# Optimization experiments

Measured on AMD Instinct MI355X. Metric: run time of the kernel, lower is better.

Reference implementation:

```python
import jax, jax.numpy as jnp
import numpy as np
from jax import lax

DIM = 512
IDIM = 1536
K = 7


def setup_inputs() -> dict:
    key = jax.random.key(0)
    ks = jax.random.split(key, 10)
    B, C, T = 16, DIM, 2048
    x = jax.random.normal(ks[0], (B, C, T), dtype=jnp.float32)
    dw_w = jax.random.normal(ks[1], (DIM, 1, K), dtype=jnp.float32) * (1.0 / np.sqrt(K))
    dw_b = jax.random.normal(ks[2], (DIM,), dtype=jnp.float32) * 0.01
    ln_g = jnp.ones((DIM,), dtype=jnp.float32)
    ln_b = jnp.zeros((DIM,), dtype=jnp.float32)
    w1 = jax.random.normal(ks[3], (IDIM, DIM), dtype=jnp.float32) * (1.0 / np.sqrt(DIM))
    b1 = jax.random.normal(ks[4], (IDIM,), dtype=jnp.float32) * 0.01
    grn_g = jax.random.normal(ks[5], (IDIM,), dtype=jnp.float32) * 0.02
    grn_b = jax.random.normal(ks[6], (IDIM,), dtype=jnp.float32) * 0.02
    w2 = jax.random.normal(ks[7], (DIM, IDIM), dtype=jnp.float32) * (1.0 / np.sqrt(IDIM))
    b2 = jax.random.normal(ks[8], (DIM,), dtype=jnp.float32) * 0.01
    return {"x": x, "dw_w": dw_w, "dw_b": dw_b, "ln_g": ln_g, "ln_b": ln_b,
            "w1": w1, "b1": b1, "grn_g": grn_g, "grn_b": grn_b, "w2": w2, "b2": b2}


def reference(x, dw_w, dw_b, ln_g, ln_b, w1, b1, grn_g, grn_b, w2, b2):
    residual = x  # [B, C, T]
    # depthwise conv1d, padding='same' style (K//2 each side)
    y = lax.conv_general_dilated(
        x, dw_w,
        window_strides=(1,),
        padding=[(K // 2, K // 2)],
        dimension_numbers=("NCH", "OIH", "NCH"),
        feature_group_count=DIM,
    ) + dw_b[None, :, None]
    y = jnp.transpose(y, (0, 2, 1))  # [B, T, C]
    # LayerNorm over channels, eps=1e-6
    mu = jnp.mean(y, axis=-1, keepdims=True)
    var = jnp.mean((y - mu) ** 2, axis=-1, keepdims=True)
    y = (y - mu) * lax.rsqrt(var + 1e-6) * ln_g + ln_b
    # pwconv1 + GELU (exact, erf-based as torch default)
    h = jnp.einsum("btc,ic->bti", y, w1) + b1  # [B, T, IDIM]
    h = jax.nn.gelu(h, approximate=False)
    # GRN: L2 norm over time axis (dim=1), mean over channels
    gx = jnp.sqrt(jnp.sum(h * h, axis=1, keepdims=True))  # [B, 1, IDIM]
    nx = gx / (jnp.mean(gx, axis=-1, keepdims=True) + 1e-6)
    h = grn_g * (h * nx) + grn_b + h
    # pwconv2
    y = jnp.einsum("bti,ci->btc", h, w2) + b2  # [B, T, C]
    y = jnp.transpose(y, (0, 2, 1))  # [B, C, T]
    return residual + y
```

## Files before the change

### kernel.cpp

```cpp
#include <hip/hip_runtime.h>
#include <math.h>

typedef unsigned short u16;
typedef unsigned int u32;
typedef __bf16 bf16x8_t __attribute__((ext_vector_type(8)));
typedef float f32x4_t __attribute__((ext_vector_type(4)));

__device__ __forceinline__ u16 f2bf(float f) {
  __bf16 b = (__bf16)f;
  return __builtin_bit_cast(u16, b);
}

__device__ __forceinline__ void gld16(const void* g, void* l) {
  __builtin_amdgcn_global_load_lds(
      (const __attribute__((address_space(1))) void*)g,
      (__attribute__((address_space(3))) void*)l, 16, 0, 0);
}

__device__ __forceinline__ float gelu_f(float v) {
  float z = 0.7978845608028654f * v * fmaf(0.044715f, v * v, 1.0f);
  float t = __builtin_amdgcn_exp2f(2.8853900817779268f * z);
  float r = __builtin_amdgcn_rcpf(t + 1.0f);
  return v - v * r;
}

__device__ __forceinline__ int swz8(int bid, int nwg) {
  int cpx = nwg >> 3;
  return (bid & 7) * cpx + (bid >> 3);
}

__global__ __launch_bounds__(256) void cast_kernel(const float* __restrict__ src,
                                                   u16* __restrict__ dst, int n) {
  int i = (blockIdx.x * 256 + threadIdx.x) * 4;
  if (i < n) {
    float4 v = *(const float4*)(src + i);
    uint2 o;
    o.x = (u32)f2bf(v.x) | ((u32)f2bf(v.y) << 16);
    o.y = (u32)f2bf(v.z) | ((u32)f2bf(v.w) << 16);
    *(uint2*)(dst + i) = o;
  }
}

__global__ __launch_bounds__(64) void b2ob_kernel(const float* __restrict__ w2,
                                                  const float* __restrict__ grn_b,
                                                  const float* __restrict__ b2,
                                                  float* __restrict__ out) {
  int c = blockIdx.x;
  int l = threadIdx.x;
  float p = 0.f;
  for (int i = l; i < 1536; i += 64) p += grn_b[i] * w2[(size_t)c * 1536 + i];
  #pragma unroll
  for (int s = 32; s; s >>= 1) p += __shfl_xor(p, s);
  if (l == 0) out[c] = b2[c] + p;
}

__global__ __launch_bounds__(512, 4) void conv_ln_kernel(const float* __restrict__ X,
                                                         const float* __restrict__ Wd,
                                                         const float* __restrict__ bd,
                                                         const float* __restrict__ lng,
                                                         const float* __restrict__ lnb,
                                                         u16* __restrict__ Y) {
  __shared__ float ystage[16 * 516];
  __shared__ float mu_s[16], rs_s[16];

  const int c = threadIdx.x;
  const int b = blockIdx.y;
  const int t0 = blockIdx.x * 64;

  const float* xr = X + ((size_t)b * 512 + c) * 2048;
  float wr[7];
  #pragma unroll
  for (int k = 0; k < 7; ++k) wr[k] = Wd[c * 7 + k];
  const float bdv = bd[c];
  const float lg = lng[c];
  const float lb = lnb[c];

  for (int ch = 0; ch < 4; ++ch) {
    const int tc0 = t0 + ch * 16;
    const int g = tc0 - 4;
    float w[24];
    if (g >= 0 && g + 24 <= 2048) {
      #pragma unroll
      for (int q = 0; q < 6; ++q) {
        float4 v = *(const float4*)(xr + g + q * 4);
        w[q * 4 + 0] = v.x; w[q * 4 + 1] = v.y;
        w[q * 4 + 2] = v.z; w[q * 4 + 3] = v.w;
      }
    } else {
      #pragma unroll
      for (int j = 0; j < 24; ++j) {
        int tt = g + j;
        w[j] = (tt >= 0 && tt < 2048) ? xr[tt] : 0.f;
      }
    }
    float outv[16];
    #pragma unroll
    for (int i = 0; i < 16; ++i) {
      float a = bdv;
      #pragma unroll
      for (int k = 0; k < 7; ++k) a = fmaf(w[i + 1 + k], wr[k], a);
      outv[i] = a;
      ystage[i * 516 + c] = a;
    }
    __syncthreads();
    {
      int r = c >> 5, cl = c & 31;
      float s = 0.f, q = 0.f;
      #pragma unroll
      for (int k = 0; k < 16; ++k) {
        float v = ystage[r * 516 + cl + k * 32];
        s += v; q += v * v;
      }
      #pragma unroll
      for (int m = 16; m; m >>= 1) { s += __shfl_xor(s, m); q += __shfl_xor(q, m); }
      if (cl == 0) {
        float mu = s * (1.f / 512.f);
        float var = q * (1.f / 512.f) - mu * mu;
        mu_s[r] = mu;
        rs_s[r] = rsqrtf(var + 1e-6f);
      }
    }
    __syncthreads();
    #pragma unroll
    for (int i = 0; i < 16; ++i) {
      float v = (outv[i] - mu_s[i]) * rs_s[i] * lg + lb;
      Y[(size_t)(b * 2048 + tc0 + i) * 512 + c] = f2bf(v);
    }
  }
}

__global__ __launch_bounds__(256) void grn_kernel(const float* __restrict__ gsum,
                                                  const float* __restrict__ grn_g,
                                                  float* __restrict__ svec) {
  __shared__ float red[256];
  int b = blockIdx.x, tid = threadIdx.x;
  float gx[6];
  float part = 0.f;
  #pragma unroll
  for (int it = 0; it < 6; ++it) {
    int i = it * 256 + tid;
    gx[it] = sqrtf(gsum[b * 1536 + i]);
    part += gx[it];
  }
  red[tid] = part;
  __syncthreads();
  for (int s = 128; s; s >>= 1) {
    if (tid < s) red[tid] += red[tid + s];
    __syncthreads();
  }
  float inv = 1.0f / (red[0] * (1.f / 1536.f) + 1e-6f);
  #pragma unroll
  for (int it = 0; it < 6; ++it) {
    int i = it * 256 + tid;
    svec[b * 1536 + i] = 1.0f + grn_g[i] * gx[it] * inv;
  }
}

__global__ __launch_bounds__(256) void w2s_kernel(const float* __restrict__ w2,
                                                  const float* __restrict__ svec,
                                                  u16* __restrict__ out) {
  size_t e0 = ((size_t)blockIdx.x * 256 + threadIdx.x) * 8;
  int i = (int)(e0 % 1536);
  size_t bc = e0 / 1536;
  int b = (int)(bc >> 9);
  size_t widx = (bc & 511) * 1536 + i;
  float4 wa = *(const float4*)(w2 + widx);
  float4 wb = *(const float4*)(w2 + widx + 4);
  float4 sa = *(const float4*)(svec + b * 1536 + i);
  float4 sb = *(const float4*)(svec + b * 1536 + i + 4);
  uint4 o;
  o.x = (u32)f2bf(wa.x * sa.x) | ((u32)f2bf(wa.y * sa.y) << 16);
  o.y = (u32)f2bf(wa.z * sa.z) | ((u32)f2bf(wa.w * sa.w) << 16);
  o.z = (u32)f2bf(wb.x * sb.x) | ((u32)f2bf(wb.y * sb.y) << 16);
  o.w = (u32)f2bf(wb.z * sb.z) | ((u32)f2bf(wb.w * sb.w) << 16);
  *(uint4*)(out + e0) = o;
}

template<int KD>
__device__ __forceinline__ void gemm_kloop(const u16* __restrict__ Ag,
                                           const u16* __restrict__ Bg,
                                           u16* lds, int NT,
                                           f32x4_t (&acc)[4][4]) {
  const int tid = threadIdx.x;
  const int l = tid & 63, l15 = l & 15, lq = l >> 4;
  const int w = tid >> 6;
  const int wm = w >> 1, wn = w & 1;
  const int rin = tid >> 3;
  const int cs = ((tid & 7) ^ (rin & 7)) << 3;

  auto STAGE = [&](int buf, int kt) {
    u16* lA = lds + buf * 16384;
    u16* lB = lA + 8192;
    #pragma unroll
    for (int c = 0; c < 4; ++c) {
      gld16(Ag + (size_t)(c * 32 + rin) * KD + kt + cs, lA + (c * 32 + w * 8) * 64);
      gld16(Bg + (size_t)(c * 32 + rin) * KD + kt + cs, lB + (c * 32 + w * 8) * 64);
    }
  };

  STAGE(0, 0);
  __syncthreads();

  for (int S = 0; S < NT; ++S) {
    const int cur = S & 1;
    if (S + 1 < NT) STAGE(cur ^ 1, (S + 1) * 64);
    u16* lA = lds + cur * 16384;
    u16* lB = lA + 8192;
    bf16x8_t af[4][2], bf[4][2];
    #pragma unroll
    for (int f = 0; f < 4; ++f) {
      const int Ra = wm * 64 + f * 16 + l15;
      const int Rb = wn * 64 + f * 16 + l15;
      #pragma unroll
      for (int kk = 0; kk < 2; ++kk) {
        af[f][kk] = *(const bf16x8_t*)(lA + Ra * 64 + (((kk * 4 + lq) ^ (Ra & 7)) << 3));
        bf[f][kk] = *(const bf16x8_t*)(lB + Rb * 64 + (((kk * 4 + lq) ^ (Rb & 7)) << 3));
      }
    }
    #pragma unroll
    for (int i = 0; i < 4; ++i)
      #pragma unroll
      for (int j = 0; j < 4; ++j)
        #pragma unroll
        for (int kk = 0; kk < 2; ++kk)
          acc[i][j] = __builtin_amdgcn_mfma_f32_16x16x32_bf16(af[i][kk], bf[j][kk], acc[i][j], 0, 0, 0);
    __syncthreads();
  }
}

__global__ __launch_bounds__(256) void gemm1_kernel(const u16* __restrict__ A,
                                                    const u16* __restrict__ Bw,
                                                    const float* __restrict__ b1,
                                                    u16* __restrict__ H,
                                                    float* __restrict__ gsum) {
  extern __shared__ __align__(16) u16 lds[];
  const int tid = threadIdx.x;
  const int l = tid & 63, l15 = l & 15, lq = l >> 4;
  const int w = tid >> 6, wm = w >> 1, wn = w & 1;
  const int wg = swz8(blockIdx.x, 3072);
  const int ntile = wg % 12, mtile = wg / 12;
  const int m0 = mtile * 128, n0 = ntile * 128;
  const int bidx = m0 >> 11;

  f32x4_t acc[4][4];
  #pragma unroll
  for (int i = 0; i < 4; ++i)
    #pragma unroll
    for (int j = 0; j < 4; ++j) {
      f32x4_t z = {0.f, 0.f, 0.f, 0.f};
      acc[i][j] = z;
    }

  gemm_kloop<512>(A + (size_t)m0 * 512, Bw + (size_t)n0 * 512, lds, 8, acc);

  float bj[4];
  #pragma unroll
  for (int nf = 0; nf < 4; ++nf) bj[nf] = b1[n0 + wn * 64 + nf * 16 + l15];

  float ss[4] = {0.f, 0.f, 0.f, 0.f};
  #pragma unroll
  for (int mf = 0; mf < 4; ++mf) {
    const int lr = wm * 64 + mf * 16 + lq * 4;
    #pragma unroll
    for (int nf = 0; nf < 4; ++nf) {
      const int cl = wn * 64 + nf * 16 + l15;
      #pragma unroll
      for (int r = 0; r < 4; ++r) {
        float g = gelu_f(acc[mf][nf][r] + bj[nf]);
        ss[nf] += g * g;
        lds[(lr + r) * 130 + cl] = f2bf(g);
      }
    }
  }
  #pragma unroll
  for (int nf = 0; nf < 4; ++nf) {
    float v = ss[nf];
    v += __shfl_xor(v, 16);
    v += __shfl_xor(v, 32);
    if (lq == 0) atomicAdd(&gsum[bidx * 1536 + n0 + wn * 64 + nf * 16 + l15], v);
  }
  __syncthreads();
  #pragma unroll
  for (int it = 0; it < 8; ++it) {
    int idx = it * 256 + tid;
    int row = idx >> 4, ch = idx & 15;
    uint4 v = *(const uint4*)(lds + row * 130 + ch * 8);
    *(uint4*)(H + (size_t)(m0 + row) * 1536 + n0 + ch * 8) = v;
  }
}

__global__ __launch_bounds__(256) void gemm2_kernel(const u16* __restrict__ Hm,
                                                    const u16* __restrict__ W2s,
                                                    const float* __restrict__ b2ob,
                                                    const float* __restrict__ X,
                                                    float* __restrict__ Out) {
  extern __shared__ __align__(16) u16 lds[];
  const int tid = threadIdx.x;
  const int l = tid & 63, l15 = l & 15, lq = l >> 4;
  const int w = tid >> 6, wm = w >> 1, wn = w & 1;
  const int wg = swz8(blockIdx.x, 1024);
  const int ntile = wg & 3, mtile = wg >> 2;
  const int m0 = mtile * 128, n0 = ntile * 128;
  const int bidx = m0 >> 11, t0 = m0 & 2047;

  f32x4_t acc[4][4];
  #pragma unroll
  for (int i = 0; i < 4; ++i)
    #pragma unroll
    for (int j = 0; j < 4; ++j) {
      f32x4_t z = {0.f, 0.f, 0.f, 0.f};
      acc[i][j] = z;
    }

  gemm_kloop<1536>(Hm + (size_t)m0 * 1536,
                   W2s + ((size_t)bidx * 512 + n0) * 1536, lds, 24, acc);

  float* st = (float*)lds;
  for (int half = 0; half < 2; ++half) {
    __syncthreads();
    if (wm == half) {
      #pragma unroll
      for (int mf = 0; mf < 4; ++mf) {
        const int lr = mf * 16 + lq * 4;
        #pragma unroll
        for (int nf = 0; nf < 4; ++nf) {
          const int cl = wn * 64 + nf * 16 + l15;
          #pragma unroll
          for (int r = 0; r < 4; ++r)
            st[(lr + r) * 129 + cl] = acc[mf][nf][r];
        }
      }
    }
    __syncthreads();
    const size_t obase = ((size_t)bidx * 512 + n0) * 2048 + (size_t)(t0 + half * 64 + l);
    #pragma unroll
    for (int cc = 0; cc < 32; ++cc) {
      const int c = w * 32 + cc;
      float v = st[l * 129 + c] + b2ob[n0 + c];
      size_t oi = obase + (size_t)c * 2048;
      Out[oi] = v + X[oi];
    }
  }
}

extern "C" void kernel_launch(void* const* d_in, const int* in_sizes, int n_in,
                              void* d_out, int out_size, void* d_ws, size_t ws_size,
                              hipStream_t stream) {
  const float* x     = (const float*)d_in[0];
  const float* dw_w  = (const float*)d_in[1];
  const float* dw_b  = (const float*)d_in[2];
  const float* ln_g  = (const float*)d_in[3];
  const float* ln_b  = (const float*)d_in[4];
  const float* w1    = (const float*)d_in[5];
  const float* b1    = (const float*)d_in[6];
  const float* grn_g = (const float*)d_in[7];
  const float* grn_b = (const float*)d_in[8];
  const float* w2    = (const float*)d_in[9];
  const float* b2    = (const float*)d_in[10];
  float* out = (float*)d_out;

  u16* y_ln = (u16*)d_ws;
  u16* w2s  = y_ln;
  u16* h    = y_ln + (size_t)32768 * 512;
  u16* w1b  = h + (size_t)32768 * 1536;
  float* gsum = (float*)(w1b + (size_t)1536 * 512);
  float* svec = gsum + 16 * 1536;
  float* b2ob = svec + 16 * 1536;

  (void)hipFuncSetAttribute((const void*)gemm1_kernel,
                            hipFuncAttributeMaxDynamicSharedMemorySize, 65536);
  (void)hipFuncSetAttribute((const void*)gemm2_kernel,
                            hipFuncAttributeMaxDynamicSharedMemorySize, 65536);

  hipMemsetAsync(gsum, 0, 16 * 1536 * sizeof(float), stream);
  cast_kernel<<<768, 256, 0, stream>>>(w1, w1b, 1536 * 512);
  b2ob_kernel<<<512, 64, 0, stream>>>(w2, grn_b, b2, b2ob);
  conv_ln_kernel<<<dim3(32, 16), 512, 0, stream>>>(x, dw_w, dw_b, ln_g, ln_b, y_ln);
  gemm1_kernel<<<3072, 256, 65536, stream>>>(y_ln, w1b, b1, h, gsum);
  grn_kernel<<<16, 256, 0, stream>>>(gsum, grn_g, svec);
  w2s_kernel<<<6144, 256, 0, stream>>>(w2, svec, w2s);
  gemm2_kernel<<<1024, 256, 65536, stream>>>(h, w2s, b2ob, x, out);
}
```

Before: 227.3 us.

## Load GEMM A operand directly into registers and halve LDS footprint

Result: slower. 321.1 us (median of 2 runs) (+41.3%).

```diff
diff --git a/kernel.cpp b/kernel.cpp
--- a/kernel.cpp
+++ b/kernel.cpp
@@ -188,34 +188,41 @@
   const int rin = tid >> 3;
   const int cs = ((tid & 7) ^ (rin & 7)) << 3;
 
-  auto STAGE = [&](int buf, int kt) {
-    u16* lA = lds + buf * 16384;
-    u16* lB = lA + 8192;
-    #pragma unroll
-    for (int c = 0; c < 4; ++c) {
-      gld16(Ag + (size_t)(c * 32 + rin) * KD + kt + cs, lA + (c * 32 + w * 8) * 64);
+  const u16* Aw = Ag + (size_t)(wm * 64 + l15) * KD + lq * 8;
+
+  auto STAGE_B = [&](int buf, int kt) {
+    u16* lB = lds + buf * 8192;
+    #pragma unroll
+    for (int c = 0; c < 4; ++c)
       gld16(Bg + (size_t)(c * 32 + rin) * KD + kt + cs, lB + (c * 32 + w * 8) * 64);
-    }
   };
-
-  STAGE(0, 0);
+  auto LOAD_A = [&](bf16x8_t (&ar)[4][2], int kt) {
+    #pragma unroll
+    for (int f = 0; f < 4; ++f)
+      #pragma unroll
+      for (int kk = 0; kk < 2; ++kk)
+        ar[f][kk] = *(const bf16x8_t*)(Aw + (size_t)(f * 16) * KD + kt + kk * 32);
+  };
+
+  bf16x8_t aP[4][2], aQ[4][2];
+  STAGE_B(0, 0);
+  LOAD_A(aP, 0);
   __syncthreads();
 
-  for (int S = 0; S < NT; ++S) {
-    const int cur = S & 1;
-    if (S + 1 < NT) STAGE(cur ^ 1, (S + 1) * 64);
-    u16* lA = lds + cur * 16384;
-    u16* lB = lA + 8192;
-    bf16x8_t af[4][2], bf[4][2];
-    #pragma unroll
-    for (int f = 0; f < 4; ++f) {
-      const int Ra = wm * 64 + f * 16 + l15;
-      const int Rb = wn * 64 + f * 16 + l15;
-      #pragma unroll
-      for (int kk = 0; kk < 2; ++kk) {
-        af[f][kk] = *(const bf16x8_t*)(lA + Ra * 64 + (((kk * 4 + lq) ^ (Ra & 7)) << 3));
-        bf[f][kk] = *(const bf16x8_t*)(lB + Rb * 64 + (((kk * 4 + lq) ^ (Rb & 7)) << 3));
-      }
+  auto STEP = [&](int S, int cur, bf16x8_t (&aC)[4][2], bf16x8_t (&aN)[4][2]) {
+    const bool pf = (S + 1 < NT);
+    if (pf) {
+      STAGE_B(cur ^ 1, (S + 1) * 64);
+      LOAD_A(aN, (S + 1) * 64);
+    }
+    u16* lB = lds + cur * 8192;
+    bf16x8_t bf[4][2];
+    #pragma unroll
+    for (int g = 0; g < 4; ++g) {
+      const int Rb = wn * 64 + g * 16 + l15;
+      #pragma unroll
+      for (int kk = 0; kk < 2; ++kk)
+        bf[g][kk] = *(const bf16x8_t*)(lB + Rb * 64 + (((kk * 4 + lq) ^ (Rb & 7)) << 3));
     }
     #pragma unroll
     for (int i = 0; i < 4; ++i)
@@ -223,16 +230,21 @@
       for (int j = 0; j < 4; ++j)
         #pragma unroll
         for (int kk = 0; kk < 2; ++kk)
-          acc[i][j] = __builtin_amdgcn_mfma_f32_16x16x32_bf16(af[i][kk], bf[j][kk], acc[i][j], 0, 0, 0);
-    __syncthreads();
-  }
-}
-
-__global__ __launch_bounds__(256) void gemm1_kernel(const u16* __restrict__ A,
-                                                    const u16* __restrict__ Bw,
-                                                    const float* __restrict__ b1,
-                                                    u16* __restrict__ H,
-                                                    float* __restrict__ gsum) {
+          acc[i][j] = __builtin_amdgcn_mfma_f32_16x16x32_bf16(aC[i][kk], bf[j][kk], acc[i][j], 0, 0, 0);
+    __syncthreads();
+  };
+
+  for (int S = 0; S < NT; S += 2) {
+    STEP(S, 0, aP, aQ);
+    STEP(S + 1, 1, aQ, aP);
+  }
+}
+
+__global__ __launch_bounds__(256, 2) void gemm1_kernel(const u16* __restrict__ A,
+                                                       const u16* __restrict__ Bw,
+                                                       const float* __restrict__ b1,
+                                                       u16* __restrict__ H,
+                                                       float* __restrict__ gsum) {
   extern __shared__ __align__(16) u16 lds[];
   const int tid = threadIdx.x;
   const int l = tid & 63, l15 = l & 15, lq = l >> 4;
@@ -289,11 +301,11 @@
   }
 }
 
-__global__ __launch_bounds__(256) void gemm2_kernel(const u16* __restrict__ Hm,
-                                                    const u16* __restrict__ W2s,
-                                                    const float* __restrict__ b2ob,
-                                                    const float* __restrict__ X,
-                                                    float* __restrict__ Out) {
+__global__ __launch_bounds__(256, 2) void gemm2_kernel(const u16* __restrict__ Hm,
+                                                       const u16* __restrict__ W2s,
+                                                       const float* __restrict__ b2ob,
+                                                       const float* __restrict__ X,
+                                                       float* __restrict__ Out) {
   extern __shared__ __align__(16) u16 lds[];
   const int tid = threadIdx.x;
   const int l = tid & 63, l15 = l & 15, lq = l >> 4;
@@ -368,16 +380,16 @@
   float* b2ob = svec + 16 * 1536;
 
   (void)hipFuncSetAttribute((const void*)gemm1_kernel,
-                            hipFuncAttributeMaxDynamicSharedMemorySize, 65536);
+                            hipFuncAttributeMaxDynamicSharedMemorySize, 33536);
   (void)hipFuncSetAttribute((const void*)gemm2_kernel,
-                            hipFuncAttributeMaxDynamicSharedMemorySize, 65536);
+                            hipFuncAttributeMaxDynamicSharedMemorySize, 33536);
 
   hipMemsetAsync(gsum, 0, 16 * 1536 * sizeof(float), stream);
   cast_kernel<<<768, 256, 0, stream>>>(w1, w1b, 1536 * 512);
   b2ob_kernel<<<512, 64, 0, stream>>>(w2, grn_b, b2, b2ob);
   conv_ln_kernel<<<dim3(32, 16), 512, 0, stream>>>(x, dw_w, dw_b, ln_g, ln_b, y_ln);
-  gemm1_kernel<<<3072, 256, 65536, stream>>>(y_ln, w1b, b1, h, gsum);
+  gemm1_kernel<<<3072, 256, 33536, stream>>>(y_ln, w1b, b1, h, gsum);
   grn_kernel<<<16, 256, 0, stream>>>(gsum, grn_g, svec);
   w2s_kernel<<<6144, 256, 0, stream>>>(w2, svec, w2s);
-  gemm2_kernel<<<1024, 256, 65536, stream>>>(h, w2s, b2ob, x, out);
-}
+  gemm2_kernel<<<1024, 256, 33536, stream>>>(h, w2s, b2ob, x, out);
+}
```

## Use 256x128 tiles with 8 waves and triple-buffered LDS pipeline in both GEMMs

Applied to the files above, without the earlier changes.

Result: slower. 239.7 us (+5.4%).

```diff
diff --git a/kernel.cpp b/kernel.cpp
--- a/kernel.cpp
+++ b/kernel.cpp
@@ -5,6 +5,13 @@
 typedef unsigned int u32;
 typedef __bf16 bf16x8_t __attribute__((ext_vector_type(8)));
 typedef float f32x4_t __attribute__((ext_vector_type(4)));
+
+#define MEMF() asm volatile("" ::: "memory")
+__device__ __forceinline__ void bar() {
+  MEMF();
+  __builtin_amdgcn_s_barrier();
+  MEMF();
+}
 
 __device__ __forceinline__ u16 f2bf(float f) {
   __bf16 b = (__bf16)f;
@@ -187,35 +194,46 @@
   const int wm = w >> 1, wn = w & 1;
   const int rin = tid >> 3;
   const int cs = ((tid & 7) ^ (rin & 7)) << 3;
+  const int wb = w * 512;
 
   auto STAGE = [&](int buf, int kt) {
-    u16* lA = lds + buf * 16384;
-    u16* lB = lA + 8192;
-    #pragma unroll
-    for (int c = 0; c < 4; ++c) {
-      gld16(Ag + (size_t)(c * 32 + rin) * KD + kt + cs, lA + (c * 32 + w * 8) * 64);
-      gld16(Bg + (size_t)(c * 32 + rin) * KD + kt + cs, lB + (c * 32 + w * 8) * 64);
-    }
+    u16* lA = lds + buf * 24576;
+    u16* lB = lA + 16384;
+    #pragma unroll
+    for (int c = 0; c < 4; ++c)
+      gld16(Ag + (size_t)(c * 64 + rin) * KD + kt + cs, lA + c * 4096 + wb);
+    #pragma unroll
+    for (int c = 0; c < 2; ++c)
+      gld16(Bg + (size_t)(c * 64 + rin) * KD + kt + cs, lB + c * 4096 + wb);
   };
 
   STAGE(0, 0);
-  __syncthreads();
-
+  STAGE(1, 64);
+  asm volatile("s_waitcnt vmcnt(6)" ::: "memory");
+  bar();
+
+  int bufS = 0;
   for (int S = 0; S < NT; ++S) {
-    const int cur = S & 1;
-    if (S + 1 < NT) STAGE(cur ^ 1, (S + 1) * 64);
-    u16* lA = lds + cur * 16384;
-    u16* lB = lA + 8192;
-    bf16x8_t af[4][2], bf[4][2];
+    if (S + 2 < NT) {
+      int bn = bufS + 2; if (bn >= 3) bn -= 3;
+      STAGE(bn, (S + 2) * 64);
+    }
+    u16* lA = lds + bufS * 24576;
+    u16* lB = lA + 16384;
+    bf16x8_t af[4][2], bfr[4][2];
     #pragma unroll
     for (int f = 0; f < 4; ++f) {
       const int Ra = wm * 64 + f * 16 + l15;
-      const int Rb = wn * 64 + f * 16 + l15;
-      #pragma unroll
-      for (int kk = 0; kk < 2; ++kk) {
+      #pragma unroll
+      for (int kk = 0; kk < 2; ++kk)
         af[f][kk] = *(const bf16x8_t*)(lA + Ra * 64 + (((kk * 4 + lq) ^ (Ra & 7)) << 3));
-        bf[f][kk] = *(const bf16x8_t*)(lB + Rb * 64 + (((kk * 4 + lq) ^ (Rb & 7)) << 3));
-      }
+    }
+    #pragma unroll
+    for (int g = 0; g < 4; ++g) {
+      const int Rb = wn * 64 + g * 16 + l15;
+      #pragma unroll
+      for (int kk = 0; kk < 2; ++kk)
+        bfr[g][kk] = *(const bf16x8_t*)(lB + Rb * 64 + (((kk * 4 + lq) ^ (Rb & 7)) << 3));
     }
     #pragma unroll
     for (int i = 0; i < 4; ++i)
@@ -223,23 +241,26 @@
       for (int j = 0; j < 4; ++j)
         #pragma unroll
         for (int kk = 0; kk < 2; ++kk)
-          acc[i][j] = __builtin_amdgcn_mfma_f32_16x16x32_bf16(af[i][kk], bf[j][kk], acc[i][j], 0, 0, 0);
-    __syncthreads();
-  }
-}
-
-__global__ __launch_bounds__(256) void gemm1_kernel(const u16* __restrict__ A,
-                                                    const u16* __restrict__ Bw,
-                                                    const float* __restrict__ b1,
-                                                    u16* __restrict__ H,
-                                                    float* __restrict__ gsum) {
+          acc[i][j] = __builtin_amdgcn_mfma_f32_16x16x32_bf16(af[i][kk], bfr[j][kk], acc[i][j], 0, 0, 0);
+    if (S + 2 < NT)      { asm volatile("s_waitcnt vmcnt(6)" ::: "memory"); }
+    else if (S + 1 < NT) { asm volatile("s_waitcnt vmcnt(0)" ::: "memory"); }
+    bar();
+    bufS = (bufS == 2) ? 0 : bufS + 1;
+  }
+}
+
+__global__ __launch_bounds__(512, 2) void gemm1_kernel(const u16* __restrict__ A,
+                                                       const u16* __restrict__ Bw,
+                                                       const float* __restrict__ b1,
+                                                       u16* __restrict__ H,
+                                                       float* __restrict__ gsum) {
   extern __shared__ __align__(16) u16 lds[];
   const int tid = threadIdx.x;
   const int l = tid & 63, l15 = l & 15, lq = l >> 4;
   const int w = tid >> 6, wm = w >> 1, wn = w & 1;
-  const int wg = swz8(blockIdx.x, 3072);
+  const int wg = swz8(blockIdx.x, 1536);
   const int ntile = wg % 12, mtile = wg / 12;
-  const int m0 = mtile * 128, n0 = ntile * 128;
+  const int m0 = mtile * 256, n0 = ntile * 128;
   const int bidx = m0 >> 11;
 
   f32x4_t acc[4][4];
@@ -282,25 +303,25 @@
   __syncthreads();
   #pragma unroll
   for (int it = 0; it < 8; ++it) {
-    int idx = it * 256 + tid;
+    int idx = it * 512 + tid;
     int row = idx >> 4, ch = idx & 15;
     uint4 v = *(const uint4*)(lds + row * 130 + ch * 8);
     *(uint4*)(H + (size_t)(m0 + row) * 1536 + n0 + ch * 8) = v;
   }
 }
 
-__global__ __launch_bounds__(256) void gemm2_kernel(const u16* __restrict__ Hm,
-                                                    const u16* __restrict__ W2s,
-                                                    const float* __restrict__ b2ob,
-                                                    const float* __restrict__ X,
-                                                    float* __restrict__ Out) {
+__global__ __launch_bounds__(512, 2) void gemm2_kernel(const u16* __restrict__ Hm,
+                                                       const u16* __restrict__ W2s,
+                                                       const float* __restrict__ b2ob,
+                                                       const float* __restrict__ X,
+                                                       float* __restrict__ Out) {
   extern __shared__ __align__(16) u16 lds[];
   const int tid = threadIdx.x;
   const int l = tid & 63, l15 = l & 15, lq = l >> 4;
   const int w = tid >> 6, wm = w >> 1, wn = w & 1;
-  const int wg = swz8(blockIdx.x, 1024);
+  const int wg = swz8(blockIdx.x, 512);
   const int ntile = wg & 3, mtile = wg >> 2;
-  const int m0 = mtile * 128, n0 = ntile * 128;
+  const int m0 = mtile * 256, n0 = ntile * 128;
   const int bidx = m0 >> 11, t0 = m0 & 2047;
 
   f32x4_t acc[4][4];
@@ -316,9 +337,9 @@
                    W2s + ((size_t)bidx * 512 + n0) * 1536, lds, 24, acc);
 
   float* st = (float*)lds;
-  for (int half = 0; half < 2; ++half) {
+  for (int grp = 0; grp < 4; ++grp) {
     __syncthreads();
-    if (wm == half) {
+    if (wm == grp) {
       #pragma unroll
       for (int mf = 0; mf < 4; ++mf) {
         const int lr = mf * 16 + lq * 4;
@@ -332,10 +353,10 @@
       }
     }
     __syncthreads();
-    const size_t obase = ((size_t)bidx * 512 + n0) * 2048 + (size_t)(t0 + half * 64 + l);
-    #pragma unroll
-    for (int cc = 0; cc < 32; ++cc) {
-      const int c = w * 32 + cc;
+    const size_t obase = ((size_t)bidx * 512 + n0) * 2048 + (size_t)(t0 + grp * 64 + l);
+    #pragma unroll
+    for (int cc = 0; cc < 16; ++cc) {
+      const int c = w * 16 + cc;
       float v = st[l * 129 + c] + b2ob[n0 + c];
       size_t oi = obase + (size_t)c * 2048;
       Out[oi] = v + X[oi];
@@ -368,16 +389,16 @@
   float* b2ob = svec + 16 * 1536;
 
   (void)hipFuncSetAttribute((const void*)gemm1_kernel,
-                            hipFuncAttributeMaxDynamicSharedMemorySize, 65536);
+                            hipFuncAttributeMaxDynamicSharedMemorySize, 147456);
   (void)hipFuncSetAttribute((const void*)gemm2_kernel,
-                            hipFuncAttributeMaxDynamicSharedMemorySize, 65536);
+                            hipFuncAttributeMaxDynamicSharedMemorySize, 147456);
 
   hipMemsetAsync(gsum, 0, 16 * 1536 * sizeof(float), stream);
   cast_kernel<<<768, 256, 0, stream>>>(w1, w1b, 1536 * 512);
   b2ob_kernel<<<512, 64, 0, stream>>>(w2, grn_b, b2, b2ob);
   conv_ln_kernel<<<dim3(32, 16), 512, 0, stream>>>(x, dw_w, dw_b, ln_g, ln_b, y_ln);
-  gemm1_kernel<<<3072, 256, 65536, stream>>>(y_ln, w1b, b1, h, gsum);
+  gemm1_kernel<<<1536, 512, 147456, stream>>>(y_ln, w1b, b1, h, gsum);
   grn_kernel<<<16, 256, 0, stream>>>(gsum, grn_g, svec);
   w2s_kernel<<<6144, 256, 0, stream>>>(w2, svec, w2s);
-  gemm2_kernel<<<1024, 256, 65536, stream>>>(h, w2s, b2ob, x, out);
-}
+  gemm2_kernel<<<512, 512, 147456, stream>>>(h, w2s, b2ob, x, out);
+}
```

## Load B operand directly from global into registers and stage only A in LDS

Applied to the files above, without the earlier changes.

Result: slower. 313.5 us (+37.9%).

```diff
diff --git a/kernel.cpp b/kernel.cpp
--- a/kernel.cpp
+++ b/kernel.cpp
@@ -176,63 +176,64 @@
   *(uint4*)(out + e0) = o;
 }
 
-template<int KD>
+template<int KD, int NC>
 __device__ __forceinline__ void gemm_kloop(const u16* __restrict__ Ag,
                                            const u16* __restrict__ Bg,
-                                           u16* lds, int NT,
+                                           u16* lds,
                                            f32x4_t (&acc)[4][4]) {
   const int tid = threadIdx.x;
   const int l = tid & 63, l15 = l & 15, lq = l >> 4;
   const int w = tid >> 6;
   const int wm = w >> 1, wn = w & 1;
-  const int rin = tid >> 3;
-  const int cs = ((tid & 7) ^ (rin & 7)) << 3;
-
-  auto STAGE = [&](int buf, int kt) {
-    u16* lA = lds + buf * 16384;
-    u16* lB = lA + 8192;
-    #pragma unroll
-    for (int c = 0; c < 4; ++c) {
-      gld16(Ag + (size_t)(c * 32 + rin) * KD + kt + cs, lA + (c * 32 + w * 8) * 64);
-      gld16(Bg + (size_t)(c * 32 + rin) * KD + kt + cs, lB + (c * 32 + w * 8) * 64);
-    }
-  };
-
-  STAGE(0, 0);
-  __syncthreads();
-
-  for (int S = 0; S < NT; ++S) {
-    const int cur = S & 1;
-    if (S + 1 < NT) STAGE(cur ^ 1, (S + 1) * 64);
-    u16* lA = lds + cur * 16384;
-    u16* lB = lA + 8192;
-    bf16x8_t af[4][2], bf[4][2];
-    #pragma unroll
-    for (int f = 0; f < 4; ++f) {
-      const int Ra = wm * 64 + f * 16 + l15;
-      const int Rb = wn * 64 + f * 16 + l15;
-      #pragma unroll
-      for (int kk = 0; kk < 2; ++kk) {
-        af[f][kk] = *(const bf16x8_t*)(lA + Ra * 64 + (((kk * 4 + lq) ^ (Ra & 7)) << 3));
-        bf[f][kk] = *(const bf16x8_t*)(lB + Rb * 64 + (((kk * 4 + lq) ^ (Rb & 7)) << 3));
-      }
-    }
-    #pragma unroll
-    for (int i = 0; i < 4; ++i)
-      #pragma unroll
-      for (int j = 0; j < 4; ++j)
+  const int lrow = l >> 5;
+  const int lchunk = l & 31;
+
+  const u16* Bl = Bg + (size_t)(wn * 64 + l15) * KD + lq * 8;
+
+  for (int c = 0; c < NC; ++c) {
+    #pragma unroll
+    for (int i = 0; i < 16; ++i) {
+      const int r = w * 32 + i * 2 + lrow;
+      const int srcCol = c * 256 + ((lchunk ^ (r & 7)) << 3);
+      gld16(Ag + (size_t)r * KD + srcCol, lds + (w * 32 + i * 2) * 256);
+    }
+    __syncthreads();
+    #pragma unroll
+    for (int s = 0; s < 4; ++s) {
+      const int kb = c * 256 + s * 64;
+      bf16x8_t bfr[4][2];
+      #pragma unroll
+      for (int g = 0; g < 4; ++g)
         #pragma unroll
         for (int kk = 0; kk < 2; ++kk)
-          acc[i][j] = __builtin_amdgcn_mfma_f32_16x16x32_bf16(af[i][kk], bf[j][kk], acc[i][j], 0, 0, 0);
-    __syncthreads();
-  }
-}
-
-__global__ __launch_bounds__(256) void gemm1_kernel(const u16* __restrict__ A,
-                                                    const u16* __restrict__ Bw,
-                                                    const float* __restrict__ b1,
-                                                    u16* __restrict__ H,
-                                                    float* __restrict__ gsum) {
+          bfr[g][kk] = *(const bf16x8_t*)(Bl + (size_t)(g * 16) * KD + kb + kk * 32);
+      bf16x8_t af[4][2];
+      #pragma unroll
+      for (int f = 0; f < 4; ++f) {
+        const int Ra = wm * 64 + f * 16 + l15;
+        #pragma unroll
+        for (int kk = 0; kk < 2; ++kk) {
+          const int ck = (s * 8 + kk * 4 + lq) ^ (Ra & 7);
+          af[f][kk] = *(const bf16x8_t*)(lds + Ra * 256 + ck * 8);
+        }
+      }
+      #pragma unroll
+      for (int i = 0; i < 4; ++i)
+        #pragma unroll
+        for (int j = 0; j < 4; ++j)
+          #pragma unroll
+          for (int kk = 0; kk < 2; ++kk)
+            acc[i][j] = __builtin_amdgcn_mfma_f32_16x16x32_bf16(af[i][kk], bfr[j][kk], acc[i][j], 0, 0, 0);
+    }
+    __syncthreads();
+  }
+}
+
+__global__ __launch_bounds__(256, 2) void gemm1_kernel(const u16* __restrict__ A,
+                                                       const u16* __restrict__ Bw,
+                                                       const float* __restrict__ b1,
+                                                       u16* __restrict__ H,
+                                                       float* __restrict__ gsum) {
   extern __shared__ __align__(16) u16 lds[];
   const int tid = threadIdx.x;
   const int l = tid & 63, l15 = l & 15, lq = l >> 4;
@@ -251,7 +252,7 @@
       acc[i][j] = z;
     }
 
-  gemm_kloop<512>(A + (size_t)m0 * 512, Bw + (size_t)n0 * 512, lds, 8, acc);
+  gemm_kloop<512, 2>(A + (size_t)m0 * 512, Bw + (size_t)n0 * 512, lds, acc);
 
   float bj[4];
   #pragma unroll
@@ -289,11 +290,11 @@
   }
 }
 
-__global__ __launch_bounds__(256) void gemm2_kernel(const u16* __restrict__ Hm,
-                                                    const u16* __restrict__ W2s,
-                                                    const float* __restrict__ b2ob,
-                                                    const float* __restrict__ X,
-                                                    float* __restrict__ Out) {
+__global__ __launch_bounds__(256, 2) void gemm2_kernel(const u16* __restrict__ Hm,
+                                                       const u16* __restrict__ W2s,
+                                                       const float* __restrict__ b2ob,
+                                                       const float* __restrict__ X,
+                                                       float* __restrict__ Out) {
   extern __shared__ __align__(16) u16 lds[];
   const int tid = threadIdx.x;
   const int l = tid & 63, l15 = l & 15, lq = l >> 4;
@@ -312,8 +313,8 @@
       acc[i][j] = z;
     }
 
-  gemm_kloop<1536>(Hm + (size_t)m0 * 1536,
-                   W2s + ((size_t)bidx * 512 + n0) * 1536, lds, 24, acc);
+  gemm_kloop<1536, 6>(Hm + (size_t)m0 * 1536,
+                      W2s + ((size_t)bidx * 512 + n0) * 1536, lds, acc);
 
   float* st = (float*)lds;
   for (int half = 0; half < 2; ++half) {
```
